# Kernel tuning notes

Measured on AMD Instinct MI355X. Metric: run time of the kernel, lower is better.

## Reference

```python
import jax, jax.numpy as jnp
import numpy as np

IN_F, OUT_F, K = 512, 512, 3
UP = 1
EPS = 1e-08
LR_MUL = 1.0
PAD = (K - 1) // 2
C_EQ = LR_MUL / np.sqrt(IN_F * K * K)  # EqualizedWeight scale


def setup_inputs() -> dict:
    key = jax.random.key(0)
    k1, k2, k3, k4 = jax.random.split(key, 4)
    b, h, w = 16, 64, 64
    x = jax.random.normal(k1, (b, IN_F, h, w), dtype=jnp.float32)
    s = jax.random.uniform(k2, (b, IN_F), dtype=jnp.float32)
    weight = jax.random.normal(k3, (OUT_F, IN_F, K, K), dtype=jnp.float32)
    bias = jax.random.normal(k4, (OUT_F,), dtype=jnp.float32)
    return {"x": x, "s": s, "weight": weight, "bias": bias}


def _conv_one(xi, wi):
    # xi: [c,h,w], wi: [out,in,k,k]
    out = jax.lax.conv_general_dilated(
        xi[None], wi,
        window_strides=(1, 1),
        padding=[(PAD, PAD), (PAD, PAD)],
        dimension_numbers=("NCHW", "OIHW", "NCHW"),
    )
    return out[0]


def reference(x, s, weight, bias):
    # modulate: [b,out,in,k,k]
    w = (weight * C_EQ)[None] * s[:, None, :, None, None]
    # demodulate
    sigma_inv = jax.lax.rsqrt(jnp.sum(w * w, axis=(2, 3, 4), keepdims=True) + EPS)
    w = w * sigma_inv
    # per-sample conv (equivalent to grouped conv with groups=b)
    out = jax.vmap(_conv_one)(x, w)  # [b,out,h,w]
    out = out + (bias * LR_MUL)[None, :, None, None]
    return out
```

## Files before the change

### kernel.cpp

```cpp
#include <hip/hip_runtime.h>
#include <cstdint>

typedef unsigned short u16;
typedef __bf16 bf16x8 __attribute__((ext_vector_type(8)));
typedef float f32x4 __attribute__((ext_vector_type(4)));

#define B_    16
#define CIN   512
#define COUT  512
#define HW_   64
#define PW    66
#define XH_ELEMS ((size_t)B_*PW*PW*CIN)
#define WA_ELEMS ((size_t)B_*16*9*COUT*32)

#define WAITV(N) asm volatile("s_waitcnt vmcnt(" #N ")" ::: "memory")

__device__ __forceinline__ u16 f2bf(float f) {
  union { float f; unsigned int u; } c; c.f = f;
  unsigned int u = c.u + 0x7fffu + ((c.u >> 16) & 1u);
  return (u16)(u >> 16);
}

__device__ __forceinline__ void async16(const void* g, void* l) {
  __builtin_amdgcn_global_load_lds(
      (__attribute__((address_space(1))) unsigned int*)(uintptr_t)g,
      (__attribute__((address_space(3))) unsigned int*)(uintptr_t)l,
      16, 0, 0);
}

__global__ __launch_bounds__(256) void zero_border(u16* __restrict__ xh) {
  int g = blockIdx.x * 256 + threadIdx.x;
  if (g >= B_ * 260 * 64) return;
  int c8 = g & 63;
  int t  = g >> 6;
  int b  = t / 260;
  int p  = t - b * 260;
  int rp, cp;
  if (p < 66)       { rp = 0;      cp = p; }
  else if (p < 132) { rp = 65;     cp = p - 66; }
  else {
    int q = p - 132;
    if (q < 64) { rp = q + 1;  cp = 0; }
    else        { rp = q - 63; cp = 65; }
  }
  u16* dst = xh + ((((size_t)b * PW + rp) * PW + cp) << 9) + (c8 << 3);
  *(uint4*)dst = make_uint4(0u, 0u, 0u, 0u);
}

__global__ __launch_bounds__(256) void transpose_x(const float* __restrict__ x,
                                                   u16* __restrict__ xh) {
  __shared__ u16 tile[64][72];
  const int b  = blockIdx.z;
  const int y  = blockIdx.y;
  const int i0 = blockIdx.x * 64;
  const int t  = threadIdx.x;

  const int ciL = t >> 4;
  const int xg  = (t & 15) * 4;
#pragma unroll
  for (int u = 0; u < 4; ++u) {
    const int ci = ciL + u * 16;
    const float4 v = *(const float4*)(
        x + ((((size_t)b * CIN + i0 + ci) * HW_ + y) * HW_ + xg));
    u16* d = &tile[ci][xg];
    d[0] = f2bf(v.x); d[1] = f2bf(v.y); d[2] = f2bf(v.z); d[3] = f2bf(v.w);
  }
  __syncthreads();

  const int xx = t >> 2;
  const int cg = (t & 3) * 16;
  u16 outv[16];
#pragma unroll
  for (int u = 0; u < 16; ++u) outv[u] = tile[cg + u][xx];
  u16* dst = xh + ((((size_t)b * PW + (y + 1)) * PW + (xx + 1)) << 9) + i0 + cg;
  *(uint4*)dst       = *(uint4*)&outv[0];
  *(uint4*)(dst + 8) = *(uint4*)&outv[8];
}

__global__ __launch_bounds__(256) void sigma_kernel(const float* __restrict__ w,
                                                    const float* __restrict__ s,
                                                    float* __restrict__ sig) {
  const int o    = blockIdx.x * 4 + (threadIdx.x >> 6);
  const int lane = threadIdx.x & 63;
  const float* wrow = w + (size_t)o * (CIN * 9);

  float q[8];
#pragma unroll
  for (int j = 0; j < 8; ++j) {
    const float* wp = wrow + (lane + j * 64) * 9;
    float qq = 0.f;
#pragma unroll
    for (int t = 0; t < 9; ++t) { const float wv = wp[t]; qq += wv * wv; }
    q[j] = qq;
  }
  const float C_EQ = 1.4731391e-2f;
#pragma unroll
  for (int b = 0; b < 16; ++b) {
    const float* srow = s + (size_t)b * CIN;
    float acc = 0.f;
#pragma unroll
    for (int j = 0; j < 8; ++j) {
      const float si = srow[lane + j * 64];
      acc += si * si * q[j];
    }
#pragma unroll
    for (int off = 32; off > 0; off >>= 1) acc += __shfl_xor(acc, off, 64);
    if (lane == 0) sig[b * COUT + o] = rsqrtf(acc * (C_EQ * C_EQ) + 1e-8f);
  }
}

__global__ __launch_bounds__(256, 2) void scale_weights(const float* __restrict__ w,
                                                        const float* __restrict__ s,
                                                        const float* __restrict__ sig,
                                                        u16* __restrict__ wA) {
  __shared__ float wld[64 * 292];
  __shared__ float s2[32];
  __shared__ float si[64];

  const int tid = threadIdx.x;
  const int lin = blockIdx.x;
  const int l   = ((lin & 7) << 8) + (lin >> 3);
  const int b   = l & 15;
  const int sid = l >> 4;
  const int icc = sid & 15;
  const int oq  = sid >> 4;
  const int o0  = oq << 6;

#pragma unroll
  for (int k = 0; k < 18; ++k) {
    const int c   = k * 256 + tid;
    const int ol  = c / 72;
    const int col = c - ol * 72;
    const float4 v = *(const float4*)(
        w + ((size_t)(o0 + ol) * 512 + icc * 32) * 9 + col * 4);
    *(float4*)&wld[ol * 292 + col * 4] = v;
  }
  if (tid < 32) s2[tid] = 1.4731391e-2f * s[(size_t)b * CIN + icc * 32 + tid];
  else if (tid < 96) si[tid - 32] = sig[(size_t)b * COUT + o0 + (tid - 32)];
  __syncthreads();

  u16* base = wA + (size_t)b * (16 * 9 * COUT * 32);
#pragma unroll
  for (int tap = 0; tap < 9; ++tap) {
    const int ol = tid >> 2;
    const int g  = tid & 3;
    const float sg = si[ol];
    u16 outc[8];
#pragma unroll
    for (int kk = 0; kk < 8; ++kk) {
      const int i = g * 8 + kk;
      outc[kk] = f2bf(wld[ol * 292 + i * 9 + tap] * s2[i] * sg);
    }
    *(uint4*)(base + (((size_t)(icc * 9 + tap) * COUT) + o0 + ol) * 32 + g * 8)
        = *(uint4*)outc;
  }
}

#define AS_ELEMS (128 * 32)
#define BROWS    (6 * 66)
#define BS_ELEMS (BROWS * 32)

__device__ __forceinline__ void stage_A(const u16* __restrict__ wb,
                                        u16* dst, int phase, int o0, int tid) {
  const u16* asrc = wb + ((size_t)phase * COUT + o0) * 32;
#pragma unroll
  for (int t = 0; t < 2; ++t) {
    const int id   = t * 256 + tid;
    const int row  = id >> 2;
    const int slot = (id & 3) ^ (row & 3);
    async16(asrc + row * 32 + slot * 8, dst + id * 8);
  }
}

__device__ __forceinline__ void stage_B_slice(const u16* __restrict__ xb,
                                              u16* dst, int ic, int y0,
                                              int tid, int slice) {
  if (tid < 198) {
    const int id   = slice * 198 + tid;
    const int row  = id >> 2;
    const int slot = (id & 3) ^ (row & 3);
    async16(xb + ((size_t)y0 * PW + row) * CIN + ic * 32 + slot * 8,
            dst + id * 8);
  }
}

__global__ __launch_bounds__(256, 2) void modconv_mfma(const u16* __restrict__ xh,
                                                       const u16* __restrict__ wA,
                                                       const float* __restrict__ bias,
                                                       float* __restrict__ out) {
  __shared__ u16 As[3 * AS_ELEMS];
  __shared__ u16 Bs[2 * BS_ELEMS];

  const int tid  = threadIdx.x;
  const int lane = tid & 63;
  const int wv   = tid >> 6;
  const int l15  = lane & 15;
  const int q    = lane >> 4;
  const int sw15 = l15 & 3;

  const int lin     = blockIdx.x;
  const int logical = ((lin & 7) << 7) + (lin >> 3);
  const int yt = logical & 15;
  const int ot = (logical >> 4) & 3;
  const int b  = logical >> 6;
  const int y0 = yt << 2;
  const int o0 = ot << 7;

  const u16* xb = xh + (size_t)b * (PW * PW * CIN);
  const u16* wb = wA + (size_t)b * (16 * 9 * COUT * 32);

  f32x4 acc[8][4];
#pragma unroll
  for (int mi = 0; mi < 8; ++mi)
#pragma unroll
    for (int cg = 0; cg < 4; ++cg) acc[mi][cg] = (f32x4){0.f, 0.f, 0.f, 0.f};

#pragma unroll
  for (int sl = 0; sl < 8; ++sl) stage_B_slice(xb, Bs, 0, y0, tid, sl);
  stage_A(wb, As, 0, o0, tid);
  stage_A(wb, As + AS_ELEMS, 1, o0, tid);

  for (int ic = 0; ic < 15; ++ic) {
    const int bOff = (ic & 1) * BS_ELEMS;
    const int bNxt = BS_ELEMS - bOff;
#pragma unroll
    for (int tap = 0; tap < 9; ++tap) {
      if (tap == 0) { WAITV(2); } else { WAITV(3); }
      __builtin_amdgcn_s_barrier();
      __builtin_amdgcn_sched_barrier(0);

      const int ky = tap / 3, kx = tap % 3;
      const int aCur = (tap % 3) * AS_ELEMS;
      const int aDst = ((tap + 2) % 3) * AS_ELEMS;
      const int rbbase = (wv + ky) * 66 + kx;

      bf16x8 bfr[4];
#pragma unroll
      for (int cg = 0; cg < 4; ++cg) {
        const int rb = rbbase + cg * 16 + l15;
        bfr[cg] = *(const bf16x8*)
          &Bs[bOff + (rb << 5) + ((q ^ (rb & 3)) << 3)];
      }

      stage_A(wb, As + aDst, ic * 9 + tap + 2, o0, tid);
      if (tap < 8) stage_B_slice(xb, Bs + bNxt, ic + 1, y0, tid, tap);

      __builtin_amdgcn_s_setprio(1);
#pragma unroll
      for (int mi = 0; mi < 8; ++mi) {
        const int ra = (mi << 4) + l15;
        const bf16x8 af = *(const bf16x8*)
          &As[aCur + (ra << 5) + ((q ^ sw15) << 3)];
#pragma unroll
        for (int cg = 0; cg < 4; ++cg)
          acc[mi][cg] = __builtin_amdgcn_mfma_f32_16x16x32_bf16(
              af, bfr[cg], acc[mi][cg], 0, 0, 0);
      }
      __builtin_amdgcn_s_setprio(0);
    }
  }

  {
    const int bOff = BS_ELEMS;
#pragma unroll
    for (int tap = 0; tap < 9; ++tap) {
      if (tap < 8) { WAITV(2); } else { WAITV(0); }
      __builtin_amdgcn_s_barrier();
      __builtin_amdgcn_sched_barrier(0);

      const int ky = tap / 3, kx = tap % 3;
      const int aCur = (tap % 3) * AS_ELEMS;
      const int rbbase = (wv + ky) * 66 + kx;

      bf16x8 bfr[4];
#pragma unroll
      for (int cg = 0; cg < 4; ++cg) {
        const int rb = rbbase + cg * 16 + l15;
        bfr[cg] = *(const bf16x8*)
          &Bs[bOff + (rb << 5) + ((q ^ (rb & 3)) << 3)];
      }

      if (tap <= 6)
        stage_A(wb, As + ((tap + 2) % 3) * AS_ELEMS, 135 + tap + 2, o0, tid);

      __builtin_amdgcn_s_setprio(1);
#pragma unroll
      for (int mi = 0; mi < 8; ++mi) {
        const int ra = (mi << 4) + l15;
        const bf16x8 af = *(const bf16x8*)
          &As[aCur + (ra << 5) + ((q ^ sw15) << 3)];
#pragma unroll
        for (int cg = 0; cg < 4; ++cg)
          acc[mi][cg] = __builtin_amdgcn_mfma_f32_16x16x32_bf16(
              af, bfr[cg], acc[mi][cg], 0, 0, 0);
      }
      __builtin_amdgcn_s_setprio(0);
    }
  }

  const int y = y0 + wv;
#pragma unroll
  for (int mi = 0; mi < 8; ++mi) {
#pragma unroll
    for (int rg = 0; rg < 4; ++rg) {
      const int o = o0 + (mi << 4) + (q << 2) + rg;
      const float bv = bias[o];
      const size_t base = (((size_t)b * COUT + o) * HW_ + y) * HW_;
#pragma unroll
      for (int cg = 0; cg < 4; ++cg)
        out[base + (cg << 4) + l15] = acc[mi][cg][rg] + bv;
    }
  }
}

extern "C" void kernel_launch(void* const* d_in, const int* in_sizes, int n_in,
                              void* d_out, int out_size, void* d_ws, size_t ws_size,
                              hipStream_t stream) {
  const float* x    = (const float*)d_in[0];
  const float* s    = (const float*)d_in[1];
  const float* w    = (const float*)d_in[2];
  const float* bias = (const float*)d_in[3];
  float* out = (float*)d_out;

  u16* xh = (u16*)d_ws;
  u16* wA = xh + XH_ELEMS;
  float* sig = (float*)d_out;

  zero_border<<<(B_ * 260 * 64 + 255) / 256, 256, 0, stream>>>(xh);
  transpose_x<<<dim3(8, 64, 16), 256, 0, stream>>>(x, xh);
  sigma_kernel<<<128, 256, 0, stream>>>(w, s, sig);
  scale_weights<<<2048, 256, 0, stream>>>(w, s, sig, wA);
  modconv_mfma<<<1024, 256, 0, stream>>>(xh, wA, bias, out);
}
```

Measured before the change: 484.4 us.

## Rework preprocessing kernels: register-only transpose, per-output sigma blocks, smaller weight tiles

The x transpose now keeps everything in registers. Each thread loads 8 channel rows as float4 and writes 16-byte bf16 channel vectors, with no LDS tile or barrier. The sigma kernel now uses one block per output channel, staging the weight row in LDS and reducing across waves, which gives more parallelism. The weight-scaling kernel uses 32-output tiles, a transposed padded LDS layout to avoid bank conflicts, and twice as many blocks, at the cost of smaller 8-byte stores. Together these aim to cut the overhead of the pre-conv kernels ahead of the main MFMA conv.

```diff
diff --git a/kernel.cpp b/kernel.cpp
--- a/kernel.cpp
+++ b/kernel.cpp
@@ -49,110 +49,120 @@
 
 __global__ __launch_bounds__(256) void transpose_x(const float* __restrict__ x,
                                                    u16* __restrict__ xh) {
-  __shared__ u16 tile[64][72];
-  const int b  = blockIdx.z;
-  const int y  = blockIdx.y;
-  const int i0 = blockIdx.x * 64;
-  const int t  = threadIdx.x;
-
-  const int ciL = t >> 4;
-  const int xg  = (t & 15) * 4;
-#pragma unroll
-  for (int u = 0; u < 4; ++u) {
-    const int ci = ciL + u * 16;
-    const float4 v = *(const float4*)(
-        x + ((((size_t)b * CIN + i0 + ci) * HW_ + y) * HW_ + xg));
-    u16* d = &tile[ci][xg];
-    d[0] = f2bf(v.x); d[1] = f2bf(v.y); d[2] = f2bf(v.z); d[3] = f2bf(v.w);
-  }
-  __syncthreads();
-
-  const int xx = t >> 2;
-  const int cg = (t & 3) * 16;
-  u16 outv[16];
-#pragma unroll
-  for (int u = 0; u < 16; ++u) outv[u] = tile[cg + u][xx];
-  u16* dst = xh + ((((size_t)b * PW + (y + 1)) * PW + (xx + 1)) << 9) + i0 + cg;
-  *(uint4*)dst       = *(uint4*)&outv[0];
-  *(uint4*)(dst + 8) = *(uint4*)&outv[8];
+  const int t   = threadIdx.x;
+  const int c8  = t & 7;
+  const int xq  = (t >> 3) & 15;
+  const int y01 = t >> 7;
+  const int i0  = blockIdx.x * 64;
+  const int y   = blockIdx.y * 2 + y01;
+  const int b   = blockIdx.z;
+
+  float4 v[8];
+#pragma unroll
+  for (int k = 0; k < 8; ++k) {
+    const int ci = i0 + c8 * 8 + k;
+    v[k] = *(const float4*)(
+        x + ((((size_t)b * CIN + ci) * HW_ + y) * HW_) + xq * 4);
+  }
+#pragma unroll
+  for (int j = 0; j < 4; ++j) {
+    const int xx = xq * 4 + j;
+    u16 oc[8];
+#pragma unroll
+    for (int k = 0; k < 8; ++k) oc[k] = f2bf(v[k][j]);
+    u16* dst = xh + ((((size_t)b * PW + (y + 1)) * PW + (xx + 1)) << 9)
+                  + i0 + c8 * 8;
+    *(uint4*)dst = *(uint4*)oc;
+  }
 }
 
 __global__ __launch_bounds__(256) void sigma_kernel(const float* __restrict__ w,
                                                     const float* __restrict__ s,
                                                     float* __restrict__ sig) {
-  const int o    = blockIdx.x * 4 + (threadIdx.x >> 6);
-  const int lane = threadIdx.x & 63;
+  __shared__ float row[CIN * 9];
+  __shared__ float part[16][4];
+
+  const int o   = blockIdx.x;
+  const int tid = threadIdx.x;
+  const int wv  = tid >> 6;
+  const int lane = tid & 63;
   const float* wrow = w + (size_t)o * (CIN * 9);
 
-  float q[8];
-#pragma unroll
-  for (int j = 0; j < 8; ++j) {
-    const float* wp = wrow + (lane + j * 64) * 9;
-    float qq = 0.f;
-#pragma unroll
-    for (int t = 0; t < 9; ++t) { const float wv = wp[t]; qq += wv * wv; }
-    q[j] = qq;
-  }
+#pragma unroll
+  for (int it = 0; it < 5; ++it) {
+    const int c = it * 256 + tid;
+    if (c < 1152) *(float4*)&row[c * 4] = *(const float4*)(wrow + c * 4);
+  }
+  __syncthreads();
+
+  float q0 = 0.f, q1 = 0.f;
+#pragma unroll
+  for (int tt = 0; tt < 9; ++tt) {
+    const float a = row[(2 * tid) * 9 + tt];
+    const float c = row[(2 * tid + 1) * 9 + tt];
+    q0 += a * a; q1 += c * c;
+  }
+
   const float C_EQ = 1.4731391e-2f;
 #pragma unroll
   for (int b = 0; b < 16; ++b) {
-    const float* srow = s + (size_t)b * CIN;
-    float acc = 0.f;
-#pragma unroll
-    for (int j = 0; j < 8; ++j) {
-      const float si = srow[lane + j * 64];
-      acc += si * si * q[j];
-    }
-#pragma unroll
-    for (int off = 32; off > 0; off >>= 1) acc += __shfl_xor(acc, off, 64);
-    if (lane == 0) sig[b * COUT + o] = rsqrtf(acc * (C_EQ * C_EQ) + 1e-8f);
-  }
-}
-
-__global__ __launch_bounds__(256, 2) void scale_weights(const float* __restrict__ w,
-                                                        const float* __restrict__ s,
-                                                        const float* __restrict__ sig,
-                                                        u16* __restrict__ wA) {
-  __shared__ float wld[64 * 292];
+    const float2 sv = *(const float2*)(s + (size_t)b * CIN + 2 * tid);
+    float a = q0 * sv.x * sv.x + q1 * sv.y * sv.y;
+#pragma unroll
+    for (int off = 32; off > 0; off >>= 1) a += __shfl_xor(a, off, 64);
+    if (lane == 0) part[b][wv] = a;
+  }
+  __syncthreads();
+  if (tid < 16) {
+    const float tot = part[tid][0] + part[tid][1] + part[tid][2] + part[tid][3];
+    sig[(size_t)tid * COUT + o] = rsqrtf(tot * (C_EQ * C_EQ) + 1e-8f);
+  }
+}
+
+__global__ __launch_bounds__(256) void scale_weights(const float* __restrict__ w,
+                                                     const float* __restrict__ s,
+                                                     const float* __restrict__ sig,
+                                                     u16* __restrict__ wA) {
+  __shared__ float wld[288][33];
   __shared__ float s2[32];
-  __shared__ float si[64];
+  __shared__ float si[32];
 
   const int tid = threadIdx.x;
-  const int lin = blockIdx.x;
-  const int l   = ((lin & 7) << 8) + (lin >> 3);
-  const int b   = l & 15;
-  const int sid = l >> 4;
-  const int icc = sid & 15;
-  const int oq  = sid >> 4;
-  const int o0  = oq << 6;
-
-#pragma unroll
-  for (int k = 0; k < 18; ++k) {
-    const int c   = k * 256 + tid;
+  const int k   = blockIdx.x & 7;
+  const int j   = blockIdx.x >> 3;
+  const int oh  = (k << 1) | (j & 1);
+  const int icc = (j >> 1) & 15;
+  const int b   = j >> 5;
+  const int o0  = oh << 5;
+
+#pragma unroll
+  for (int it = 0; it < 9; ++it) {
+    const int c   = it * 256 + tid;
     const int ol  = c / 72;
     const int col = c - ol * 72;
     const float4 v = *(const float4*)(
-        w + ((size_t)(o0 + ol) * 512 + icc * 32) * 9 + col * 4);
-    *(float4*)&wld[ol * 292 + col * 4] = v;
-  }
-  if (tid < 32) s2[tid] = 1.4731391e-2f * s[(size_t)b * CIN + icc * 32 + tid];
-  else if (tid < 96) si[tid - 32] = sig[(size_t)b * COUT + o0 + (tid - 32)];
+        w + (size_t)(o0 + ol) * (CIN * 9) + icc * 288 + col * 4);
+#pragma unroll
+    for (int j2 = 0; j2 < 4; ++j2) wld[col * 4 + j2][ol] = v[j2];
+  }
+  if (tid < 32)      s2[tid] = 1.4731391e-2f * s[(size_t)b * CIN + icc * 32 + tid];
+  else if (tid < 64) si[tid - 32] = sig[(size_t)b * COUT + o0 + (tid - 32)];
   __syncthreads();
 
+  const int ol = tid >> 3;
+  const int g4 = tid & 7;
+  const float sg = si[ol];
   u16* base = wA + (size_t)b * (16 * 9 * COUT * 32);
 #pragma unroll
   for (int tap = 0; tap < 9; ++tap) {
-    const int ol = tid >> 2;
-    const int g  = tid & 3;
-    const float sg = si[ol];
-    u16 outc[8];
-#pragma unroll
-    for (int kk = 0; kk < 8; ++kk) {
-      const int i = g * 8 + kk;
-      outc[kk] = f2bf(wld[ol * 292 + i * 9 + tap] * s2[i] * sg);
+    u16 oc[4];
+#pragma unroll
+    for (int kk = 0; kk < 4; ++kk) {
+      const int ich = g4 * 4 + kk;
+      oc[kk] = f2bf(wld[ich * 9 + tap][ol] * s2[ich] * sg);
     }
-    *(uint4*)(base + (((size_t)(icc * 9 + tap) * COUT) + o0 + ol) * 32 + g * 8)
-        = *(uint4*)outc;
+    *(uint2*)(base + (((size_t)(icc * 9 + tap) * COUT) + o0 + ol) * 32 + g4 * 4)
+        = *(uint2*)oc;
   }
 }
 
@@ -327,8 +337,8 @@
   float* sig = (float*)d_out;
 
   zero_border<<<(B_ * 260 * 64 + 255) / 256, 256, 0, stream>>>(xh);
-  transpose_x<<<dim3(8, 64, 16), 256, 0, stream>>>(x, xh);
-  sigma_kernel<<<128, 256, 0, stream>>>(w, s, sig);
-  scale_weights<<<2048, 256, 0, stream>>>(w, s, sig, wA);
+  transpose_x<<<dim3(8, 32, 16), 256, 0, stream>>>(x, xh);
+  sigma_kernel<<<512, 256, 0, stream>>>(w, s, sig);
+  scale_weights<<<4096, 256, 0, stream>>>(w, s, sig, wA);
   modconv_mfma<<<1024, 256, 0, stream>>>(xh, wA, bias, out);
 }
```

Result: no change. 477.2 us (-1.5%).
